# Kernel tuning notes

Hardware: AMD Instinct MI355X
Metric: run time of the kernel (lower is better)

Reference implementation:

```python
import jax, jax.numpy as jnp
import numpy as np

TOP_K = 2
SCALING = 32.0 / 16.0  # lora_alpha / r

N, D, O = 4096, 4096, 4096   # tokens, in_features, out_features
E, H, R_RANK = 8, 3, 16      # experts, B-heads per expert, lora rank
W_SCALE = 0.02               # keep logits in a sane range


def setup_inputs() -> dict:
    key = jax.random.key(0)
    ks = jax.random.split(key, 6)
    return {
        "x": jax.random.normal(ks[0], (N, D), jnp.float32),
        "base_W": jax.random.normal(ks[1], (D, O), jnp.float32) * W_SCALE,
        "router_W": jax.random.normal(ks[2], (E, D), jnp.float32) * W_SCALE,
        "A": jax.random.normal(ks[3], (E, D, R_RANK), jnp.float32) * W_SCALE,
        "B": jax.random.normal(ks[4], (E, H, R_RANK, O), jnp.float32) * W_SCALE,
        "R": jax.random.normal(ks[5], (E, D, H), jnp.float32) * W_SCALE,
    }


def reference(x, base_W, router_W, A, B, R):
    # Base dense layer
    base = x @ base_W                                   # [N, O]
    # Expert router: softmax over experts, top-k gate renormalized
    probs = jax.nn.softmax(x @ router_W.T, axis=-1)     # [N, E]
    topv, topi = jax.lax.top_k(probs, TOP_K)            # [N, k]
    topv = topv / topv.sum(-1, keepdims=True)
    n_idx = jnp.arange(x.shape[0])[:, None]
    gate = jnp.zeros_like(probs).at[n_idx, topi].set(topv)  # dense [N, E] gate, 0 off top-k
    # Shared lora_A per expert
    a = jnp.einsum('nd,edr->ner', x, A)                 # [N, E, r]
    # Per-expert head router over lora_B heads
    head_w = jax.nn.softmax(jnp.einsum('nd,edh->neh', x, R), axis=-1)  # [N, E, H]
    # Head-weighted B projections, combined with expert gates
    delta = jnp.einsum('ner,neh,ehro,ne->no', a, head_w, B, gate)      # [N, O]
    return base + SCALING * delta
```

## Files before the change

kernel.cpp:

```cpp
#include <hip/hip_runtime.h>
#include <hip/hip_bf16.h>
#include <math.h>

typedef __bf16 bf16_t;
typedef __bf16 bf16x4_t __attribute__((ext_vector_type(4)));
typedef __bf16 bf16x8_t __attribute__((ext_vector_type(8)));
typedef float  f32x4_t  __attribute__((ext_vector_type(4)));

#define N_TOK 4096
#define D_IN  4096
#define O_OUT 4096
#define NEXP  8
#define NHEAD 3
#define RANK  16
#define KC2   384
#define PCOLS 256
#define SCALING_F 2.0f


__device__ __forceinline__ void transpose_tile(const float* __restrict__ src,
                                               bf16_t* __restrict__ dst,
                                               int Rr, int Cc, int r0, int c0,
                                               float (*tile)[65]) {
  int q  = threadIdx.x & 15;
  int r4 = threadIdx.x >> 4;
  #pragma unroll
  for (int g = 0; g < 4; ++g) {
    int r = r4 + g * 16;
    float4 v = *(const float4*)(src + (size_t)(r0 + r) * Cc + c0 + q * 4);
    tile[r][q * 4 + 0] = v.x; tile[r][q * 4 + 1] = v.y;
    tile[r][q * 4 + 2] = v.z; tile[r][q * 4 + 3] = v.w;
  }
  __syncthreads();
  #pragma unroll
  for (int g = 0; g < 4; ++g) {
    int c = r4 + g * 16;
    bf16x4_t o = { (bf16_t)tile[q * 4 + 0][c], (bf16_t)tile[q * 4 + 1][c],
                   (bf16_t)tile[q * 4 + 2][c], (bf16_t)tile[q * 4 + 3][c] };
    *(bf16x4_t*)(dst + (size_t)(c0 + c) * Rr + r0 + q * 4) = o;
  }
}

__global__ __launch_bounds__(256) void prep_kernel(const float* __restrict__ x,
                                                   const float* __restrict__ base_W,
                                                   const float* __restrict__ rw,
                                                   const float* __restrict__ A,
                                                   const float* __restrict__ B,
                                                   const float* __restrict__ Rm,
                                                   bf16_t* __restrict__ xb,
                                                   bf16_t* __restrict__ WbT,
                                                   bf16_t* __restrict__ BbT,
                                                   bf16_t* __restrict__ PabT,
                                                   int* __restrict__ gidx,
                                                   float* __restrict__ gwv) {
  __shared__ float tile[64][65];
  int b = blockIdx.x;
  if (b < 4096) {
    transpose_tile(base_W, WbT, 4096, 4096, (b & 63) * 64, (b >> 6) * 64, tile);
  } else if (b < 5120) {
    int lane = threadIdx.x & 63;
    int wv = threadIdx.x >> 6;
    int n = (b - 4096) * 4 + wv;
    const float4* xv = (const float4*)(x + (size_t)n * D_IN);
    bf16x4_t* xo = (bf16x4_t*)(xb + (size_t)n * D_IN);
    float acc[NEXP] = {0, 0, 0, 0, 0, 0, 0, 0};
    for (int d = lane; d < D_IN / 4; d += 64) {
      float4 xx = xv[d];
      bf16x4_t ob = { (bf16_t)xx.x, (bf16_t)xx.y, (bf16_t)xx.z, (bf16_t)xx.w };
      xo[d] = ob;
      #pragma unroll
      for (int e = 0; e < NEXP; ++e) {
        float4 ww = ((const float4*)(rw + (size_t)e * D_IN))[d];
        acc[e] += xx.x * ww.x + xx.y * ww.y + xx.z * ww.z + xx.w * ww.w;
      }
    }
    #pragma unroll
    for (int e = 0; e < NEXP; ++e) {
      float v = acc[e];
      #pragma unroll
      for (int o = 32; o > 0; o >>= 1) v += __shfl_down(v, o);
      acc[e] = v;
    }
    if (lane == 0) {
      int i0 = 0; float l0 = acc[0];
      #pragma unroll
      for (int e = 1; e < NEXP; ++e) if (acc[e] > l0) { l0 = acc[e]; i0 = e; }
      int i1 = -1; float l1 = -3.4e38f;
      #pragma unroll
      for (int e = 0; e < NEXP; ++e) if (e != i0 && acc[e] > l1) { l1 = acc[e]; i1 = e; }
      float w0 = 1.f / (1.f + expf(l1 - l0));
      gidx[2 * n] = i0; gidx[2 * n + 1] = i1;
      gwv[2 * n] = w0;  gwv[2 * n + 1] = 1.f - w0;
    }
  } else if (b < 5504) {
    int t = b - 5120;
    transpose_tile(B, BbT, KC2, 4096, (t % 6) * 64, (t / 6) * 64, tile);
  } else {
    int c = b - 5504;
    for (int d = threadIdx.x; d < D_IN; d += 256) {
      float v = 0.f;
      if (c < 128) {
        int e = c >> 4, r = c & 15;
        v = A[((size_t)e * D_IN + d) * RANK + r];
      } else if (c < 152) {
        int qq = c - 128; int e = qq / 3, h = qq - 3 * e;
        v = Rm[((size_t)e * D_IN + d) * NHEAD + h];
      }
      PabT[(size_t)c * D_IN + d] = (bf16_t)v;
    }
  }
}

__global__ void gating_kernel(const float* __restrict__ projP, const int* __restrict__ gidx,
                              const float* __restrict__ gwv, bf16_t* __restrict__ C2b) {
  int n = blockIdx.x;
  int c = threadIdx.x;
  int e = c / 48;
  int h = (c % 48) / 16;
  int r = c & 15;
  int i0 = gidx[2 * n], i1 = gidx[2 * n + 1];
  float g = (e == i0) ? gwv[2 * n] : (e == i1) ? gwv[2 * n + 1] : 0.f;
  float val = 0.f;
  if (g != 0.f) {
    const float* p0 = projP + (size_t)n * PCOLS;
    const size_t S = (size_t)N_TOK * PCOLS;
    #define RD(cc) (p0[(cc)] + p0[(cc) + S] + p0[(cc) + 2 * S] + p0[(cc) + 3 * S])
    float h0 = RD(128 + e * 3 + 0);
    float h1 = RD(128 + e * 3 + 1);
    float h2 = RD(128 + e * 3 + 2);
    float av = RD(e * 16 + r);
    #undef RD
    float mx = fmaxf(h0, fmaxf(h1, h2));
    float e0 = expf(h0 - mx), e1 = expf(h1 - mx), e2 = expf(h2 - mx);
    float hw = (h == 0 ? e0 : h == 1 ? e1 : e2) / (e0 + e1 + e2);
    val = SCALING_F * g * hw * av;
  }
  C2b[(size_t)n * KC2 + c] = (bf16_t)val;
}

__device__ __forceinline__ void run_kloop(f32x4_t (&acc)[4][4], bf16_t* sA, bf16_t* sB,
                                          const bf16_t* __restrict__ Ab, int lda,
                                          const bf16_t* __restrict__ Bb, int ldb, int K) {
  const int tid = threadIdx.x;
  const int lane = tid & 63;
  const int w = tid >> 6;
  const int wm = (w >> 1) * 64;
  const int wn = (w & 1) * 64;
  const int qd = lane >> 4;
  const int ln = lane & 15;
  const int sw = ln & 7;

  size_t offA[4], offB[4];
  int lo[4];
  #pragma unroll
  for (int t = 0; t < 4; ++t) {
    int c = tid + t * 256;
    int m = c >> 3, kc = (c & 7) ^ (m & 7);
    offA[t] = (size_t)m * lda + kc * 8;
    offB[t] = (size_t)m * ldb + kc * 8;
    lo[t] = c * 8;
  }
  int rowA[4], rowB[4];
  #pragma unroll
  for (int i = 0; i < 4; ++i) {
    rowA[i] = (wm + i * 16 + ln) * 64;
    rowB[i] = (wn + i * 16 + ln) * 64;
  }

  for (int k0 = 0; k0 < K; k0 += 64) {
    __syncthreads();
    #pragma unroll
    for (int t = 0; t < 4; ++t)
      __builtin_amdgcn_global_load_lds(
          (const __attribute__((address_space(1))) void*)(Ab + k0 + offA[t]),
          (__attribute__((address_space(3))) void*)(sA + lo[t]), 16, 0, 0);
    #pragma unroll
    for (int t = 0; t < 4; ++t)
      __builtin_amdgcn_global_load_lds(
          (const __attribute__((address_space(1))) void*)(Bb + k0 + offB[t]),
          (__attribute__((address_space(3))) void*)(sB + lo[t]), 16, 0, 0);
    __syncthreads();
    #pragma unroll
    for (int s = 0; s < 2; ++s) {
      bf16x8_t af[4], bfr[4];
      int kx = ((s * 4 + qd) ^ sw) * 8;
      #pragma unroll
      for (int i = 0; i < 4; ++i) af[i]  = *(const bf16x8_t*)(sA + rowA[i] + kx);
      #pragma unroll
      for (int i = 0; i < 4; ++i) bfr[i] = *(const bf16x8_t*)(sB + rowB[i] + kx);
      #pragma unroll
      for (int i = 0; i < 4; ++i)
        #pragma unroll
        for (int j = 0; j < 4; ++j)
          acc[i][j] = __builtin_amdgcn_mfma_f32_16x16x32_bf16(af[i], bfr[j], acc[i][j], 0, 0, 0);
    }
  }
}

__global__ __launch_bounds__(256) void gemm_proj_kernel(const bf16_t* __restrict__ xb,
                                                        const bf16_t* __restrict__ PabT,
                                                        float* __restrict__ projP) {
  __shared__ bf16_t sA[128 * 64];
  __shared__ bf16_t sB[128 * 64];
  int bm = blockIdx.x, bn = blockIdx.y, kz = blockIdx.z;
  f32x4_t acc[4][4] = {};
  run_kloop(acc, sA, sB,
            xb + (size_t)bm * 128 * D_IN + kz * 1024, D_IN,
            PabT + (size_t)bn * 128 * D_IN + kz * 1024, D_IN, 1024);
  const int lane = threadIdx.x & 63, w = threadIdx.x >> 6;
  const int wm = (w >> 1) * 64, wn = (w & 1) * 64, qd = lane >> 4, ln = lane & 15;
  float* Cb = projP + (size_t)kz * N_TOK * PCOLS + (size_t)bm * 128 * PCOLS + bn * 128;
  #pragma unroll
  for (int i = 0; i < 4; ++i)
    #pragma unroll
    for (int j = 0; j < 4; ++j) {
      int col = wn + j * 16 + ln;
      #pragma unroll
      for (int rg = 0; rg < 4; ++rg) {
        int row = wm + i * 16 + qd * 4 + rg;
        Cb[(size_t)row * PCOLS + col] = acc[i][j][rg];
      }
    }
}


__device__ __forceinline__ void stage256(const bf16_t* __restrict__ G, int ld, int k0,
                                         bf16_t* lbase, int tid) {
  #pragma unroll
  for (int r = 0; r < 2; ++r) {
    int s = r * 512 + tid;
    int row = s >> 2;
    int c = (s & 3) ^ ((row >> 1) & 3);
    __builtin_amdgcn_global_load_lds(
        (const __attribute__((address_space(1))) void*)(G + (size_t)row * ld + k0 + c * 8),
        (__attribute__((address_space(3))) void*)(lbase + s * 8), 16, 0, 0);
  }
}

template <int MB>
__device__ __forceinline__ void mfma16(f32x4_t (&acc)[8][4], const bf16x8_t (&af)[4],
                                       const bf16x8_t (&bv)[4]) {
  __builtin_amdgcn_s_setprio(1);
  #pragma unroll
  for (int mi = 0; mi < 4; ++mi)
    #pragma unroll
    for (int nj = 0; nj < 4; ++nj)
      acc[MB + mi][nj] =
          __builtin_amdgcn_mfma_f32_16x16x32_bf16(af[mi], bv[nj], acc[MB + mi][nj], 0, 0, 0);
  __builtin_amdgcn_s_setprio(0);
}

__device__ __forceinline__ void compute256(f32x4_t (&acc)[8][4],
                                           const bf16_t* pA, const bf16_t* pB) {
  bf16x8_t af[8], bv[4];
  #pragma unroll
  for (int nj = 0; nj < 4; ++nj) bv[nj] = *(const bf16x8_t*)(pB + nj * 512);
  #pragma unroll
  for (int mi = 0; mi < 8; ++mi) af[mi] = *(const bf16x8_t*)(pA + mi * 512);
  __builtin_amdgcn_s_setprio(1);
  #pragma unroll
  for (int mi = 0; mi < 8; ++mi)
    #pragma unroll
    for (int nj = 0; nj < 4; ++nj)
      acc[mi][nj] = __builtin_amdgcn_mfma_f32_16x16x32_bf16(af[mi], bv[nj], acc[mi][nj], 0, 0, 0);
  __builtin_amdgcn_s_setprio(0);
}

__device__ __forceinline__ void kloop256(f32x4_t (&acc)[8][4], bf16_t* sring,
                                         const bf16_t* __restrict__ A, int lda,
                                         const bf16_t* __restrict__ B, int ldb,
                                         int K, int tid, int aoff, int boff) {
  const int T = K / 32;
  #pragma unroll
  for (int t = 0; t < 3; ++t) {
    stage256(A, lda, t * 32, sring + t * 16384, tid);
    stage256(B, ldb, t * 32, sring + t * 16384 + 8192, tid);
  }
  for (int t = 0; t < T - 3; ++t) {
    const int k3 = (t + 3) * 32;
    const int s3 = (t + 3) & 3;
    const int sc = t & 3;
    stage256(A, lda, k3, sring + s3 * 16384, tid);
    asm volatile("s_waitcnt vmcnt(10)" ::: "memory");
    __builtin_amdgcn_s_barrier();
    __builtin_amdgcn_sched_barrier(0);
    const bf16_t* pA = sring + sc * 16384 + aoff;
    const bf16_t* pB = sring + sc * 16384 + 8192 + boff;
    bf16x8_t bv[4], a0[4], a1[4];
    #pragma unroll
    for (int nj = 0; nj < 4; ++nj) bv[nj] = *(const bf16x8_t*)(pB + nj * 512);
    #pragma unroll
    for (int mi = 0; mi < 4; ++mi) a0[mi] = *(const bf16x8_t*)(pA + mi * 512);
    stage256(B, ldb, k3, sring + s3 * 16384 + 8192, tid);
    asm volatile("s_waitcnt lgkmcnt(0)" ::: "memory");
    __builtin_amdgcn_sched_barrier(0);
    mfma16<0>(acc, a0, bv);
    #pragma unroll
    for (int mi = 0; mi < 4; ++mi) a1[mi] = *(const bf16x8_t*)(pA + (4 + mi) * 512);
    __builtin_amdgcn_sched_barrier(0);
    __builtin_amdgcn_s_barrier();
    __builtin_amdgcn_sched_barrier(0);
    asm volatile("s_waitcnt lgkmcnt(0)" ::: "memory");
    __builtin_amdgcn_sched_barrier(0);
    mfma16<4>(acc, a1, bv);
    __builtin_amdgcn_sched_barrier(0);
    __builtin_amdgcn_s_barrier();
    __builtin_amdgcn_sched_barrier(0);
  }
  #pragma unroll 1
  for (int t = T - 3; t < T; ++t) {
    const int rem = T - t;
    if (rem == 3)      asm volatile("s_waitcnt vmcnt(8)" ::: "memory");
    else if (rem == 2) asm volatile("s_waitcnt vmcnt(4)" ::: "memory");
    else               asm volatile("s_waitcnt vmcnt(0)" ::: "memory");
    __builtin_amdgcn_s_barrier();
    __builtin_amdgcn_sched_barrier(0);
    compute256(acc, sring + (t & 3) * 16384 + aoff, sring + (t & 3) * 16384 + 8192 + boff);
    __builtin_amdgcn_sched_barrier(0);
    __builtin_amdgcn_s_barrier();
    __builtin_amdgcn_sched_barrier(0);
  }
}

__global__ __launch_bounds__(512, 1) void gemm_fused256(const bf16_t* __restrict__ xb,
                                                        const bf16_t* __restrict__ WbT,
                                                        const bf16_t* __restrict__ C2b,
                                                        const bf16_t* __restrict__ BbT,
                                                        float* __restrict__ out) {
  __shared__ __align__(16) bf16_t sring[4 * 16384];
  const int tid = threadIdx.x;
  const int lane = tid & 63;
  const int w = tid >> 6;
  const int wm = w >> 2;
  const int wn = w & 3;
  const int qd = lane >> 4;
  const int ln = lane & 15;
  const int swz8 = ((qd ^ ((ln >> 1) & 3)) << 3);

  int b = blockIdx.x;
  int sw = (b & 7) * 32 + (b >> 3);
  int bm = sw >> 4, bn = sw & 15;

  const int aoff = (wm * 128 + ln) * 32 + swz8;
  const int boff = (wn * 64 + ln) * 32 + swz8;

  f32x4_t acc[8][4] = {};

  kloop256(acc, sring, xb  + (size_t)bm * 256 * D_IN, D_IN,
                       WbT + (size_t)bn * 256 * D_IN, D_IN, D_IN, tid, aoff, boff);
  kloop256(acc, sring, C2b + (size_t)bm * 256 * KC2,  KC2,
                       BbT + (size_t)bn * 256 * KC2,  KC2,  KC2,  tid, aoff, boff);

  float* Cb = out + (size_t)(bm * 256 + wm * 128) * O_OUT + bn * 256 + wn * 64;
  #pragma unroll
  for (int mi = 0; mi < 8; ++mi)
    #pragma unroll
    for (int nj = 0; nj < 4; ++nj)
      #pragma unroll
      for (int rg = 0; rg < 4; ++rg)
        Cb[(size_t)(mi * 16 + qd * 4 + rg) * O_OUT + nj * 16 + ln] = acc[mi][nj][rg];
}

extern "C" void kernel_launch(void* const* d_in, const int* in_sizes, int n_in,
                              void* d_out, int out_size, void* d_ws, size_t ws_size,
                              hipStream_t stream) {
  const float* x       = (const float*)d_in[0];
  const float* base_W  = (const float*)d_in[1];
  const float* routerW = (const float*)d_in[2];
  const float* A       = (const float*)d_in[3];
  const float* B       = (const float*)d_in[4];
  const float* Rm      = (const float*)d_in[5];
  float* out = (float*)d_out;
  char* ws = (char*)d_ws;

  bf16_t* xb   = (bf16_t*)(ws);
  bf16_t* WbT  = (bf16_t*)(ws + 33554432);
  bf16_t* PabT = (bf16_t*)(ws + 67108864);
  bf16_t* BbT  = (bf16_t*)(ws + 69206016);
  bf16_t* C2b  = (bf16_t*)(ws + 72351744);
  int*    gidx = (int*)   (ws + 75497472);
  float*  gwv  = (float*) (ws + 75530240);
  float*  projP = out;

  prep_kernel<<<5760, 256, 0, stream>>>(x, base_W, routerW, A, B, Rm,
                                        xb, WbT, BbT, PabT, gidx, gwv);
  gemm_proj_kernel<<<dim3(32, 2, 4), 256, 0, stream>>>(xb, PabT, projP);
  gating_kernel<<<4096, 384, 0, stream>>>(projP, gidx, gwv, C2b);
  gemm_fused256<<<dim3(256), 512, 0, stream>>>(xb, WbT, C2b, BbT, out);
}
```

Baseline: 363.8 us.

## Rework main GEMM to 64-wide K double buffer, widen split-K, vectorize transpose stores

```diff
diff --git a/kernel.cpp b/kernel.cpp
--- a/kernel.cpp
+++ b/kernel.cpp
@@ -15,6 +15,7 @@
 #define RANK  16
 #define KC2   384
 #define PCOLS 256
+#define NKZ   8
 #define SCALING_F 2.0f
 
 
@@ -32,12 +33,15 @@
     tile[r][q * 4 + 2] = v.z; tile[r][q * 4 + 3] = v.w;
   }
   __syncthreads();
-  #pragma unroll
-  for (int g = 0; g < 4; ++g) {
-    int c = r4 + g * 16;
-    bf16x4_t o = { (bf16_t)tile[q * 4 + 0][c], (bf16_t)tile[q * 4 + 1][c],
-                   (bf16_t)tile[q * 4 + 2][c], (bf16_t)tile[q * 4 + 3][c] };
-    *(bf16x4_t*)(dst + (size_t)(c0 + c) * Rr + r0 + q * 4) = o;
+  int j  = threadIdx.x & 7;
+  int cc = threadIdx.x >> 3;
+  #pragma unroll
+  for (int h = 0; h < 2; ++h) {
+    int c = cc + h * 32;
+    bf16x8_t o;
+    #pragma unroll
+    for (int i = 0; i < 8; ++i) o[i] = (bf16_t)tile[j * 8 + i][c];
+    *(bf16x8_t*)(dst + (size_t)(c0 + c) * Rr + r0 + j * 8) = o;
   }
 }
 
@@ -124,12 +128,15 @@
   if (g != 0.f) {
     const float* p0 = projP + (size_t)n * PCOLS;
     const size_t S = (size_t)N_TOK * PCOLS;
-    #define RD(cc) (p0[(cc)] + p0[(cc) + S] + p0[(cc) + 2 * S] + p0[(cc) + 3 * S])
-    float h0 = RD(128 + e * 3 + 0);
-    float h1 = RD(128 + e * 3 + 1);
-    float h2 = RD(128 + e * 3 + 2);
-    float av = RD(e * 16 + r);
-    #undef RD
+    float h0 = 0.f, h1 = 0.f, h2 = 0.f, av = 0.f;
+    #pragma unroll
+    for (int z = 0; z < NKZ; ++z) {
+      const float* pz = p0 + (size_t)z * S;
+      h0 += pz[128 + e * 3 + 0];
+      h1 += pz[128 + e * 3 + 1];
+      h2 += pz[128 + e * 3 + 2];
+      av += pz[e * 16 + r];
+    }
     float mx = fmaxf(h0, fmaxf(h1, h2));
     float e0 = expf(h0 - mx), e1 = expf(h1 - mx), e2 = expf(h2 - mx);
     float hw = (h == 0 ? e0 : h == 1 ? e1 : e2) / (e0 + e1 + e2);
@@ -205,8 +212,8 @@
   int bm = blockIdx.x, bn = blockIdx.y, kz = blockIdx.z;
   f32x4_t acc[4][4] = {};
   run_kloop(acc, sA, sB,
-            xb + (size_t)bm * 128 * D_IN + kz * 1024, D_IN,
-            PabT + (size_t)bn * 128 * D_IN + kz * 1024, D_IN, 1024);
+            xb + (size_t)bm * 128 * D_IN + kz * 512, D_IN,
+            PabT + (size_t)bn * 128 * D_IN + kz * 512, D_IN, 512);
   const int lane = threadIdx.x & 63, w = threadIdx.x >> 6;
   const int wm = (w >> 1) * 64, wn = (w & 1) * 64, qd = lane >> 4, ln = lane & 15;
   float* Cb = projP + (size_t)kz * N_TOK * PCOLS + (size_t)bm * 128 * PCOLS + bn * 128;
@@ -224,17 +231,15 @@
 }
 
 
-__device__ __forceinline__ void stage256(const bf16_t* __restrict__ G, int ld, int k0,
-                                         bf16_t* lbase, int tid) {
-  #pragma unroll
-  for (int r = 0; r < 2; ++r) {
-    int s = r * 512 + tid;
-    int row = s >> 2;
-    int c = (s & 3) ^ ((row >> 1) & 3);
+#define SLOT 32768
+
+__device__ __forceinline__ void stage4(const bf16_t* __restrict__ G, int k0,
+                                       bf16_t* lbase, const size_t (&g)[4], int tid) {
+  #pragma unroll
+  for (int i = 0; i < 4; ++i)
     __builtin_amdgcn_global_load_lds(
-        (const __attribute__((address_space(1))) void*)(G + (size_t)row * ld + k0 + c * 8),
-        (__attribute__((address_space(3))) void*)(lbase + s * 8), 16, 0, 0);
-  }
+        (const __attribute__((address_space(1))) void*)(G + g[i] + k0),
+        (__attribute__((address_space(3))) void*)(lbase + (i * 512 + tid) * 8), 16, 0, 0);
 }
 
 template <int MB>
@@ -250,76 +255,86 @@
   __builtin_amdgcn_s_setprio(0);
 }
 
-__device__ __forceinline__ void compute256(f32x4_t (&acc)[8][4],
-                                           const bf16_t* pA, const bf16_t* pB) {
-  bf16x8_t af[8], bv[4];
-  #pragma unroll
-  for (int nj = 0; nj < 4; ++nj) bv[nj] = *(const bf16x8_t*)(pB + nj * 512);
-  #pragma unroll
-  for (int mi = 0; mi < 8; ++mi) af[mi] = *(const bf16x8_t*)(pA + mi * 512);
-  __builtin_amdgcn_s_setprio(1);
-  #pragma unroll
-  for (int mi = 0; mi < 8; ++mi)
-    #pragma unroll
-    for (int nj = 0; nj < 4; ++nj)
-      acc[mi][nj] = __builtin_amdgcn_mfma_f32_16x16x32_bf16(af[mi], bv[nj], acc[mi][nj], 0, 0, 0);
-  __builtin_amdgcn_s_setprio(0);
-}
-
-__device__ __forceinline__ void kloop256(f32x4_t (&acc)[8][4], bf16_t* sring,
-                                         const bf16_t* __restrict__ A, int lda,
-                                         const bf16_t* __restrict__ B, int ldb,
-                                         int K, int tid, int aoff, int boff) {
-  const int T = K / 32;
-  #pragma unroll
-  for (int t = 0; t < 3; ++t) {
-    stage256(A, lda, t * 32, sring + t * 16384, tid);
-    stage256(B, ldb, t * 32, sring + t * 16384 + 8192, tid);
-  }
-  for (int t = 0; t < T - 3; ++t) {
-    const int k3 = (t + 3) * 32;
-    const int s3 = (t + 3) & 3;
-    const int sc = t & 3;
-    stage256(A, lda, k3, sring + s3 * 16384, tid);
-    asm volatile("s_waitcnt vmcnt(10)" ::: "memory");
-    __builtin_amdgcn_s_barrier();
-    __builtin_amdgcn_sched_barrier(0);
-    const bf16_t* pA = sring + sc * 16384 + aoff;
-    const bf16_t* pB = sring + sc * 16384 + 8192 + boff;
-    bf16x8_t bv[4], a0[4], a1[4];
-    #pragma unroll
-    for (int nj = 0; nj < 4; ++nj) bv[nj] = *(const bf16x8_t*)(pB + nj * 512);
-    #pragma unroll
-    for (int mi = 0; mi < 4; ++mi) a0[mi] = *(const bf16x8_t*)(pA + mi * 512);
-    stage256(B, ldb, k3, sring + s3 * 16384 + 8192, tid);
-    asm volatile("s_waitcnt lgkmcnt(0)" ::: "memory");
-    __builtin_amdgcn_sched_barrier(0);
-    mfma16<0>(acc, a0, bv);
-    #pragma unroll
-    for (int mi = 0; mi < 4; ++mi) a1[mi] = *(const bf16x8_t*)(pA + (4 + mi) * 512);
-    __builtin_amdgcn_sched_barrier(0);
-    __builtin_amdgcn_s_barrier();
-    __builtin_amdgcn_sched_barrier(0);
-    asm volatile("s_waitcnt lgkmcnt(0)" ::: "memory");
-    __builtin_amdgcn_sched_barrier(0);
-    mfma16<4>(acc, a1, bv);
-    __builtin_amdgcn_sched_barrier(0);
-    __builtin_amdgcn_s_barrier();
-    __builtin_amdgcn_sched_barrier(0);
-  }
-  #pragma unroll 1
-  for (int t = T - 3; t < T; ++t) {
-    const int rem = T - t;
-    if (rem == 3)      asm volatile("s_waitcnt vmcnt(8)" ::: "memory");
-    else if (rem == 2) asm volatile("s_waitcnt vmcnt(4)" ::: "memory");
-    else               asm volatile("s_waitcnt vmcnt(0)" ::: "memory");
-    __builtin_amdgcn_s_barrier();
-    __builtin_amdgcn_sched_barrier(0);
-    compute256(acc, sring + (t & 3) * 16384 + aoff, sring + (t & 3) * 16384 + 8192 + boff);
-    __builtin_amdgcn_sched_barrier(0);
-    __builtin_amdgcn_s_barrier();
-    __builtin_amdgcn_sched_barrier(0);
-  }
+__device__ __forceinline__ void substep64(f32x4_t (&acc)[8][4], const bf16_t* pA,
+                                          const bf16_t* pB, int kx) {
+  bf16x8_t bv[4], a0[4], a1[4];
+  #pragma unroll
+  for (int nj = 0; nj < 4; ++nj) bv[nj] = *(const bf16x8_t*)(pB + nj * 1024 + kx);
+  #pragma unroll
+  for (int mi = 0; mi < 4; ++mi) a0[mi] = *(const bf16x8_t*)(pA + mi * 1024 + kx);
+  mfma16<0>(acc, a0, bv);
+  #pragma unroll
+  for (int mi = 0; mi < 4; ++mi) a1[mi] = *(const bf16x8_t*)(pA + (4 + mi) * 1024 + kx);
+  mfma16<4>(acc, a1, bv);
+}
+
+template <int SC>
+__device__ __forceinline__ void tbody64(f32x4_t (&acc)[8][4], bf16_t* sring,
+                                        const bf16_t* __restrict__ A,
+                                        const bf16_t* __restrict__ B, int k1,
+                                        const size_t (&gA)[4], const size_t (&gB)[4],
+                                        int aoff, int boff, int kx0, int kx1, int tid) {
+  stage4(A, k1, sring + (SC ^ 1) * SLOT, gA, tid);
+  asm volatile("s_waitcnt vmcnt(4)" ::: "memory");
+  __builtin_amdgcn_s_barrier();
+  const bf16_t* pA = sring + SC * SLOT + aoff;
+  const bf16_t* pB = sring + SC * SLOT + 16384 + boff;
+  bf16x8_t bv[4], a0[4], a1[4];
+  #pragma unroll
+  for (int nj = 0; nj < 4; ++nj) bv[nj] = *(const bf16x8_t*)(pB + nj * 1024 + kx0);
+  #pragma unroll
+  for (int mi = 0; mi < 4; ++mi) a0[mi] = *(const bf16x8_t*)(pA + mi * 1024 + kx0);
+  stage4(B, k1, sring + (SC ^ 1) * SLOT + 16384, gB, tid);
+  mfma16<0>(acc, a0, bv);
+  #pragma unroll
+  for (int mi = 0; mi < 4; ++mi) a1[mi] = *(const bf16x8_t*)(pA + (4 + mi) * 1024 + kx0);
+  mfma16<4>(acc, a1, bv);
+  __builtin_amdgcn_s_barrier();
+  substep64(acc, pA, pB, kx1);
+  __builtin_amdgcn_sched_barrier(0);
+  __builtin_amdgcn_s_barrier();
+}
+
+__device__ __forceinline__ void tail64(f32x4_t (&acc)[8][4], const bf16_t* slotbase,
+                                       int aoff, int boff, int kx0, int kx1) {
+  asm volatile("s_waitcnt vmcnt(0)" ::: "memory");
+  __builtin_amdgcn_s_barrier();
+  const bf16_t* pA = slotbase + aoff;
+  const bf16_t* pB = slotbase + 16384 + boff;
+  substep64(acc, pA, pB, kx0);
+  __builtin_amdgcn_s_barrier();
+  substep64(acc, pA, pB, kx1);
+  __builtin_amdgcn_sched_barrier(0);
+  __builtin_amdgcn_s_barrier();
+}
+
+__device__ __forceinline__ void kloop64(f32x4_t (&acc)[8][4], bf16_t* sring,
+                                        const bf16_t* __restrict__ A, int lda,
+                                        const bf16_t* __restrict__ B, int ldb,
+                                        int K, int tid, int aoff, int boff,
+                                        int kx0, int kx1) {
+  size_t gA[4], gB[4];
+  #pragma unroll
+  for (int i = 0; i < 4; ++i) {
+    int s = i * 512 + tid;
+    int row = s >> 3;
+    int c = (s & 7) ^ (row & 7);
+    gA[i] = (size_t)row * lda + c * 8;
+    gB[i] = (size_t)row * ldb + c * 8;
+  }
+  const int T = K / 64;
+  stage4(A, 0, sring, gA, tid);
+  stage4(B, 0, sring + 16384, gB, tid);
+  int t = 0;
+  for (; t + 1 < T - 1; t += 2) {
+    tbody64<0>(acc, sring, A, B, (t + 1) * 64, gA, gB, aoff, boff, kx0, kx1, tid);
+    tbody64<1>(acc, sring, A, B, (t + 2) * 64, gA, gB, aoff, boff, kx0, kx1, tid);
+  }
+  for (; t < T - 1; ++t) {
+    if (t & 1) tbody64<1>(acc, sring, A, B, (t + 1) * 64, gA, gB, aoff, boff, kx0, kx1, tid);
+    else       tbody64<0>(acc, sring, A, B, (t + 1) * 64, gA, gB, aoff, boff, kx0, kx1, tid);
+  }
+  tail64(acc, sring + ((T - 1) & 1) * SLOT, aoff, boff, kx0, kx1);
 }
 
 __global__ __launch_bounds__(512, 1) void gemm_fused256(const bf16_t* __restrict__ xb,
@@ -327,7 +342,7 @@
                                                         const bf16_t* __restrict__ C2b,
                                                         const bf16_t* __restrict__ BbT,
                                                         float* __restrict__ out) {
-  __shared__ __align__(16) bf16_t sring[4 * 16384];
+  __shared__ __align__(16) bf16_t sring[2 * SLOT];
   const int tid = threadIdx.x;
   const int lane = tid & 63;
   const int w = tid >> 6;
@@ -335,21 +350,22 @@
   const int wn = w & 3;
   const int qd = lane >> 4;
   const int ln = lane & 15;
-  const int swz8 = ((qd ^ ((ln >> 1) & 3)) << 3);
 
   int b = blockIdx.x;
   int sw = (b & 7) * 32 + (b >> 3);
   int bm = sw >> 4, bn = sw & 15;
 
-  const int aoff = (wm * 128 + ln) * 32 + swz8;
-  const int boff = (wn * 64 + ln) * 32 + swz8;
+  const int aoff = (wm * 128 + ln) * 64;
+  const int boff = (wn * 64 + ln) * 64;
+  const int kx0 = ((qd) ^ (ln & 7)) * 8;
+  const int kx1 = ((4 + qd) ^ (ln & 7)) * 8;
 
   f32x4_t acc[8][4] = {};
 
-  kloop256(acc, sring, xb  + (size_t)bm * 256 * D_IN, D_IN,
-                       WbT + (size_t)bn * 256 * D_IN, D_IN, D_IN, tid, aoff, boff);
-  kloop256(acc, sring, C2b + (size_t)bm * 256 * KC2,  KC2,
-                       BbT + (size_t)bn * 256 * KC2,  KC2,  KC2,  tid, aoff, boff);
+  kloop64(acc, sring, xb  + (size_t)bm * 256 * D_IN, D_IN,
+                      WbT + (size_t)bn * 256 * D_IN, D_IN, D_IN, tid, aoff, boff, kx0, kx1);
+  kloop64(acc, sring, C2b + (size_t)bm * 256 * KC2,  KC2,
+                      BbT + (size_t)bn * 256 * KC2,  KC2,  KC2,  tid, aoff, boff, kx0, kx1);
 
   float* Cb = out + (size_t)(bm * 256 + wm * 128) * O_OUT + bn * 256 + wn * 64;
   #pragma unroll
@@ -384,7 +400,7 @@
 
   prep_kernel<<<5760, 256, 0, stream>>>(x, base_W, routerW, A, B, Rm,
                                         xb, WbT, BbT, PabT, gidx, gwv);
-  gemm_proj_kernel<<<dim3(32, 2, 4), 256, 0, stream>>>(xb, PabT, projP);
+  gemm_proj_kernel<<<dim3(32, 2, NKZ), 256, 0, stream>>>(xb, PabT, projP);
   gating_kernel<<<4096, 384, 0, stream>>>(projP, gidx, gwv, C2b);
   gemm_fused256<<<dim3(256), 512, 0, stream>>>(xb, WbT, C2b, BbT, out);
 }
```

After: 356.2 us. 1.02x faster.
